# Optimization experiments

Hardware: AMD Instinct MI355X
Metric: run time of the kernel (lower is better)

Reference implementation:

```python
import jax, jax.numpy as jnp
import numpy as np

N_NODES = 100000
N_EDGES = 1600000
N_GRAPHS = 2048
HID = 64
IN_F = 14
N_CLS = 2
EPS = 1e-5


def _gcn_conv(x, row, col, w_edge, W, b, n_nodes):
    # PyG GCNConv with add_self_loops=True, normalize=True.
    xw = x @ W  # [N, out]
    # degree on target nodes, self-loop contributes weight 1
    deg = jnp.zeros((n_nodes,), x.dtype).at[col].add(w_edge) + 1.0
    dinv = deg ** -0.5
    norm = dinv[row] * w_edge * dinv[col]  # [E]
    out = jnp.zeros_like(xw).at[col].add(norm[:, None] * xw[row])
    out = out + (dinv * dinv)[:, None] * xw  # self-loop term
    return out + b


def _bn_relu(x, gamma, beta):
    mean = jnp.mean(x, axis=0)
    var = jnp.var(x, axis=0)  # biased, as PyTorch BN training normalization
    y = gamma * (x - mean) * jax.lax.rsqrt(var + EPS) + beta
    return jax.nn.relu(y)


def setup_inputs() -> dict:
    key = jax.random.key(0)
    ks = jax.random.split(key, 8)
    x = jax.random.normal(ks[0], (N_NODES, IN_F), dtype=jnp.float32)
    edge_index = jax.random.randint(ks[1], (2, N_EDGES), 0, N_NODES, dtype=jnp.int64)
    batch = jnp.sort(jax.random.randint(ks[2], (N_NODES,), 0, N_GRAPHS, dtype=jnp.int64))
    edge_weight = jnp.ones((N_EDGES,), dtype=jnp.float32)
    def lin(k, fi, fo):
        s = 1.0 / np.sqrt(fi)
        kw, kb = jax.random.split(k)
        return (jax.random.uniform(kw, (fi, fo), jnp.float32, -s, s),
                jax.random.uniform(kb, (fo,), jnp.float32, -s, s))
    W1, b1 = lin(ks[3], IN_F, HID)
    W2, b2 = lin(ks[4], HID, HID)
    W3, b3 = lin(ks[5], HID, HID)
    fcW, fcb = lin(ks[6], HID, N_CLS)
    g = jnp.ones((HID,), jnp.float32)
    z = jnp.zeros((HID,), jnp.float32)
    return {
        "x": x, "edge_index": edge_index, "batch": batch, "edge_weight": edge_weight,
        "W1": W1, "b1": b1, "W2": W2, "b2": b2, "W3": W3, "b3": b3,
        "g1": g, "bt1": z, "g2": g, "bt2": z, "g3": g, "bt3": z,
        "fcW": fcW, "fcb": fcb,
    }


def reference(x, edge_index, batch, edge_weight, W1, b1, W2, b2, W3, b3,
              g1, bt1, g2, bt2, g3, bt3, fcW, fcb):
    row, col = edge_index[0], edge_index[1]
    n = x.shape[0]
    h = _bn_relu(_gcn_conv(x, row, col, edge_weight, W1, b1, n), g1, bt1)
    h = _bn_relu(_gcn_conv(h, row, col, edge_weight, W2, b2, n), g2, bt2)
    h = _bn_relu(_gcn_conv(h, row, col, edge_weight, W3, b3, n), g3, bt3)
    node_embs = h  # dropout p=0 is identity
    graph_emb = jax.ops.segment_sum(node_embs, batch, num_segments=N_GRAPHS)
    out = graph_emb @ fcW + fcb
    return (out, node_embs, graph_emb)
```

## Files before the change

kernel.cpp:

```cpp
#include <hip/hip_runtime.h>
#include <hip/hip_fp16.h>

#define N_NODES 100000
#define N_EDGES 1600000
#define EMAX2   2000000
#define N_GRAPHS 2048
#define HID 64
#define IN_F 14
#define N_CLS 2
#define EPS 1e-5f

#define BSHIFT 9
#define NBUCK 196
#define ABLOCKS 256
#define CHUNK (N_EDGES / ABLOCKS)

#define NBLK2 128
#define NCHUNK2 ((N_NODES + NBLK2 - 1) / NBLK2)

typedef _Float16 half_t;
typedef _Float16 half8 __attribute__((ext_vector_type(8)));
typedef float f32x4 __attribute__((ext_vector_type(4)));

#define GSTRIDE ((size_t)N_NODES * 16)


__global__ __launch_bounds__(256) void histA_kernel(const int* __restrict__ col,
                                                    int* __restrict__ histG,
                                                    int* __restrict__ bsumA,
                                                    float* __restrict__ gemb,
                                                    float* __restrict__ stats3) {
    __shared__ int hl[NBUCK];
    for (int i = threadIdx.x; i < NBUCK; i += 256) hl[i] = 0;
    for (int k = threadIdx.x; k < 512; k += 256)
        gemb[(size_t)blockIdx.x * 512 + k] = 0.f;
    if (blockIdx.x == 0 && threadIdx.x < 384) stats3[threadIdx.x] = 0.f;
    __syncthreads();
    int e0 = blockIdx.x * CHUNK;
    for (int e = e0 + threadIdx.x; e < e0 + CHUNK; e += 256)
        atomicAdd(&hl[col[e] >> BSHIFT], 1);
    __syncthreads();
    for (int i = threadIdx.x; i < NBUCK; i += 256) {
        int v = hl[i];
        histG[i * ABLOCKS + blockIdx.x] = v;
        atomicAdd(&bsumA[i], v);
    }
}

__global__ __launch_bounds__(256) void scanS3_kernel(int* __restrict__ histG,
                                                     const int* __restrict__ bsumA,
                                                     int* __restrict__ bsumX,
                                                     int* __restrict__ ptr) {
    __shared__ int ls[256], bs[256];
    int t = threadIdx.x;
    int rawB = (blockIdx.x < NBUCK) ? bsumA[blockIdx.x] : 0;
    bs[t] = (t < NBUCK) ? bsumA[t] : 0;
    int idx = blockIdx.x * 256 + t;
    int v = histG[idx];
    ls[t] = v;
    __syncthreads();
    for (int off = 1; off < 256; off <<= 1) {
        int x = ls[t];
        int y = bs[t];
        if (t >= off) { x += ls[t - off]; y += bs[t - off]; }
        __syncthreads();
        ls[t] = x; bs[t] = y;
        __syncthreads();
    }
    int bexcl = bs[blockIdx.x] - rawB;
    histG[idx] = ls[t] - v + bexcl;
    if (t == 0) bsumX[blockIdx.x] = bexcl;
    if (blockIdx.x == 0 && t == 0) ptr[N_NODES] = N_EDGES;
}

__global__ __launch_bounds__(256) void scatterA_kernel(const int* __restrict__ row,
                                                       const int* __restrict__ col,
                                                       const float* __restrict__ w,
                                                       const int* __restrict__ histG,
                                                       int2* __restrict__ EA) {
    __shared__ int cur[NBUCK];
    for (int i = threadIdx.x; i < NBUCK; i += 256)
        cur[i] = histG[i * ABLOCKS + blockIdx.x];
    __syncthreads();
    int e0 = blockIdx.x * CHUNK;
    for (int e = e0 + threadIdx.x; e < e0 + CHUNK; e += 256) {
        int c = col[e];
        int r = row[e];
        int fx = (int)__float2uint_rn(w[e] * 8192.0f);
        int pos = atomicAdd(&cur[c >> BSHIFT], 1);
        EA[pos] = make_int2(r, (fx << 17) | c);
    }
}

__global__ __launch_bounds__(256) void bucketA_kernel(const int2* __restrict__ EA,
                                                      const int* __restrict__ bsumX,
                                                      int* __restrict__ ptr,
                                                      float* __restrict__ dinv) {
    __shared__ int hist[512], wsum[512];
    int b = blockIdx.x;
    int beg = bsumX[b];
    int end = (b == NBUCK - 1) ? N_EDGES : bsumX[b + 1];
    int i0 = threadIdx.x, i1 = threadIdx.x + 256;
    hist[i0] = 0; hist[i1] = 0;
    wsum[i0] = 0; wsum[i1] = 0;
    __syncthreads();
    for (int e = beg + threadIdx.x; e < end; e += 256) {
        int2 ed = EA[e];
        int c9 = ed.y & 511;
        atomicAdd(&hist[c9], 1);
        atomicAdd(&wsum[c9], (int)((unsigned int)ed.y >> 17));
    }
    __syncthreads();
    int cnt0 = hist[i0], cnt1 = hist[i1];
    for (int off = 1; off < 512; off <<= 1) {
        int v0 = hist[i0], v1 = hist[i1];
        int a0 = (i0 >= off) ? hist[i0 - off] : 0;
        int a1 = (i1 >= off) ? hist[i1 - off] : 0;
        __syncthreads();
        hist[i0] = v0 + a0;
        hist[i1] = v1 + a1;
        __syncthreads();
    }
    int excl0 = hist[i0] - cnt0, excl1 = hist[i1] - cnt1;
    int col0 = (b << BSHIFT) + i0, col1 = (b << BSHIFT) + i1;
    if (col0 < N_NODES) {
        ptr[col0] = beg + excl0;
        dinv[col0] = rsqrtf(1.0f + (float)wsum[i0] * (1.0f / 8192.0f));
    }
    if (col1 < N_NODES) {
        ptr[col1] = beg + excl1;
        dinv[col1] = rsqrtf(1.0f + (float)wsum[i1] * (1.0f / 8192.0f));
    }
}


__global__ __launch_bounds__(256) void histD_kernel(const int* __restrict__ ptr,
                                                    int* __restrict__ histD,
                                                    int* __restrict__ rowTot) {
    __shared__ int hl[2048];
    for (int i = threadIdx.x; i < 2048; i += 256) hl[i] = 0;
    __syncthreads();
    int n0 = blockIdx.x * NCHUNK2;
    int n1 = n0 + NCHUNK2; if (n1 > N_NODES) n1 = N_NODES;
    for (int n = n0 + threadIdx.x; n < n1; n += 256) {
        int d = ptr[n + 1] - ptr[n];
        if (d > 255) d = 255;
        atomicAdd(&hl[((threadIdx.x & 7) << 8) + d], 1);
    }
    __syncthreads();
    int s = 0;
#pragma unroll
    for (int c = 0; c < 8; c++) s += hl[(c << 8) + threadIdx.x];
    histD[threadIdx.x * NBLK2 + blockIdx.x] = s;
    atomicAdd(&rowTot[threadIdx.x], s);
}

__global__ __launch_bounds__(128) void scanD3_kernel(int* __restrict__ histD,
                                                     const int* __restrict__ rowTot,
                                                     int* __restrict__ nodeExcl,
                                                     int* __restrict__ edgeExcl,
                                                     int* __restrict__ ptrS) {
    __shared__ int ls[128], sa[256], sb[256];
    int t = threadIdx.x;
    int bin = blockIdx.x;
    int c0 = rowTot[t], c1 = rowTot[t + 128];
    sa[t] = c0;           sa[t + 128] = c1;
    sb[t] = c0 * ((t + 3) & ~3);
    sb[t + 128] = c1 * ((t + 131) & ~3);
    int idx = bin * NBLK2 + t;
    int v = histD[idx];
    ls[t] = v;
    __syncthreads();
    for (int off = 1; off < 256; off <<= 1) {
        int a0 = sa[t], a1 = sa[t + 128];
        int b0 = sb[t], b1 = sb[t + 128];
        int x0 = (t >= off) ? sa[t - off] : 0;
        int x1 = (t + 128 >= off) ? sa[t + 128 - off] : 0;
        int y0 = (t >= off) ? sb[t - off] : 0;
        int y1 = (t + 128 >= off) ? sb[t + 128 - off] : 0;
        __syncthreads();
        sa[t] = a0 + x0; sa[t + 128] = a1 + x1;
        sb[t] = b0 + y0; sb[t + 128] = b1 + y1;
        __syncthreads();
    }
    for (int off = 1; off < 128; off <<= 1) {
        int x = ls[t];
        if (t >= off) x += ls[t - off];
        __syncthreads();
        ls[t] = x;
        __syncthreads();
    }
    int nE = sa[bin] - rowTot[bin];
    histD[idx] = ls[t] - v + nE;
    if (bin == 0) {
        nodeExcl[t] = sa[t] - rowTot[t];
        nodeExcl[t + 128] = sa[t + 128] - rowTot[t + 128];
        edgeExcl[t] = sb[t] - rowTot[t] * ((t + 3) & ~3);
        edgeExcl[t + 128] = sb[t + 128] - rowTot[t + 128] * ((t + 131) & ~3);
        if (t == 127) ptrS[N_NODES] = sb[255];
    }
}

__global__ __launch_bounds__(256) void scatterD_kernel(const int* __restrict__ ptr,
                                                       const int* __restrict__ histD,
                                                       const int* __restrict__ nodeExcl,
                                                       const int* __restrict__ edgeExcl,
                                                       int* __restrict__ perm,
                                                       int* __restrict__ ptrS,
                                                       int* __restrict__ newbase,
                                                       unsigned int* __restrict__ srcoff,
                                                       half_t* __restrict__ normh) {
    __shared__ int cur[256];
    cur[threadIdx.x] = histD[threadIdx.x * NBLK2 + blockIdx.x];
    __syncthreads();
    int n0 = blockIdx.x * NCHUNK2;
    int n1 = n0 + NCHUNK2; if (n1 > N_NODES) n1 = N_NODES;
    for (int n = n0 + threadIdx.x; n < n1; n += 256) {
        int d = ptr[n + 1] - ptr[n];
        if (d > 255) d = 255;
        int dpad = (d + 3) & ~3;
        int pos = atomicAdd(&cur[d], 1);
        int ebase = edgeExcl[d] + (pos - nodeExcl[d]) * dpad;
        perm[pos] = n;
        ptrS[pos] = ebase;
        newbase[n] = ebase;
        for (int k = d; k < dpad; k++) {
            srcoff[ebase + k] = 0u;
            normh[ebase + k] = (half_t)0.f;
        }
    }
}

__global__ __launch_bounds__(256) void bucketB_kernel(const int2* __restrict__ EA,
                                                      const int* __restrict__ bsumX,
                                                      const int* __restrict__ newbase,
                                                      unsigned int* __restrict__ srcoff,
                                                      half_t* __restrict__ normh) {
    __shared__ int cur[512];
    int b = blockIdx.x;
    int beg = bsumX[b];
    int end = (b == NBUCK - 1) ? N_EDGES : bsumX[b + 1];
    int i0 = threadIdx.x, i1 = threadIdx.x + 256;
    int col0 = (b << BSHIFT) + i0, col1 = (b << BSHIFT) + i1;
    cur[i0] = (col0 < N_NODES) ? newbase[col0] : 0;
    cur[i1] = (col1 < N_NODES) ? newbase[col1] : 0;
    __syncthreads();
    for (int e = beg + threadIdx.x; e < end; e += 256) {
        int2 ed = EA[e];
        int c = ed.y & 0x1ffff;
        float w = (float)((unsigned int)ed.y >> 17) * (1.0f / 8192.0f);
        int pos = atomicAdd(&cur[c & 511], 1);
        srcoff[pos] = (unsigned int)ed.x << 5;
        normh[pos] = (half_t)w;
    }
}


template <int K>
__global__ __launch_bounds__(256) void gemm_kernel(const float* __restrict__ h,
                                                   const float* __restrict__ W,
                                                   const float* __restrict__ dinv,
                                                   half_t* __restrict__ xw, int n_nodes) {
    int f = threadIdx.x & 63;
    float wcol[K];
#pragma unroll
    for (int k = 0; k < K; k++) wcol[k] = W[k * HID + f];
    half_t* xg = xw + (size_t)(f >> 4) * GSTRIDE + (f & 15);
    int wave = (blockIdx.x * blockDim.x + threadIdx.x) >> 6;
    int nwaves = (gridDim.x * blockDim.x) >> 6;
    for (int n = wave; n < n_nodes; n += nwaves) {
        const float* hr = h + (size_t)n * K;
        float acc = 0.f;
#pragma unroll
        for (int k = 0; k < K; k++) acc += hr[k] * wcol[k];
        xg[(size_t)n * 16] = (half_t)(acc * dinv[n]);
    }
}

__global__ __launch_bounds__(256) void gemm_bn_mfma_kernel(const half_t* __restrict__ h,
                                                           const float* __restrict__ W,
                                                           const float* __restrict__ stats,
                                                           const float* __restrict__ gamma,
                                                           const float* __restrict__ beta,
                                                           const float* __restrict__ dinv,
                                                           half_t* __restrict__ xw, int n_nodes) {
    __shared__ float sc_s[HID], sh_s[HID];
    if (threadIdx.x < 64) {
        float mean = stats[threadIdx.x] * (1.0f / N_NODES);
        float var = stats[64 + threadIdx.x] * (1.0f / N_NODES) - mean * mean;
        float sc = gamma[threadIdx.x] * rsqrtf(var + EPS);
        sc_s[threadIdx.x] = sc;
        sh_s[threadIdx.x] = beta[threadIdx.x] - mean * sc;
    }
    __syncthreads();
    int lane = threadIdx.x & 63;
    int col16 = lane & 15;
    int quad = lane >> 4;

    float scA[2][8], shA[2][8];
#pragma unroll
    for (int kh = 0; kh < 2; kh++)
#pragma unroll
        for (int j = 0; j < 8; j++) {
            int k = kh * 32 + quad * 8 + j;
            scA[kh][j] = sc_s[k];
            shA[kh][j] = sh_s[k];
        }

    half8 bfrag[4][2];
#pragma unroll
    for (int t = 0; t < 4; t++)
#pragma unroll
        for (int kh = 0; kh < 2; kh++)
#pragma unroll
            for (int j = 0; j < 8; j++) {
                int k = kh * 32 + quad * 8 + j;
                bfrag[t][kh][j] = (half_t)W[k * HID + t * 16 + col16];
            }

    int wave = (blockIdx.x * blockDim.x + threadIdx.x) >> 6;
    int nwaves = (gridDim.x * blockDim.x) >> 6;
    int ntiles = n_nodes >> 4;
    for (int tIdx = wave; tIdx < ntiles; tIdx += nwaves) {
        int n0 = tIdx << 4;
        half8 afrag[2];
#pragma unroll
        for (int kh = 0; kh < 2; kh++) {
            int k0 = kh * 32 + quad * 8;
            const half_t* hp = h + (size_t)(k0 >> 4) * GSTRIDE
                                 + (size_t)(n0 + col16) * 16 + (k0 & 15);
            half8 raw = *(const half8*)hp;
#pragma unroll
            for (int j = 0; j < 8; j++) {
                float v = (float)raw[j] * scA[kh][j] + shA[kh][j];
                afrag[kh][j] = (half_t)fmaxf(v, 0.f);
            }
        }
        f32x4 acc[4];
#pragma unroll
        for (int t = 0; t < 4; t++) {
            f32x4 z = {0.f, 0.f, 0.f, 0.f};
            acc[t] = __builtin_amdgcn_mfma_f32_16x16x32_f16(afrag[0], bfrag[t][0], z, 0, 0, 0);
            acc[t] = __builtin_amdgcn_mfma_f32_16x16x32_f16(afrag[1], bfrag[t][1], acc[t], 0, 0, 0);
        }
        f32x4 dv = *(const f32x4*)(dinv + n0 + quad * 4);
#pragma unroll
        for (int t = 0; t < 4; t++) {
            half_t* xg = xw + (size_t)t * GSTRIDE;
#pragma unroll
            for (int r = 0; r < 4; r++) {
                int rowi = n0 + quad * 4 + r;
                xg[(size_t)rowi * 16 + col16] = (half_t)(acc[t][r] * dv[r]);
            }
        }
    }
}

__global__ __launch_bounds__(256) void gather_stats_kernel(const int* __restrict__ ptrS,
                                                           const int* __restrict__ perm,
                                                           const unsigned int* __restrict__ srcoff,
                                                           const unsigned int* __restrict__ normu,
                                                           const half_t* __restrict__ xw,
                                                           const float* __restrict__ dinv,
                                                           const float* __restrict__ b,
                                                           half_t* __restrict__ hp,
                                                           float* __restrict__ stats,
                                                           int n_nodes) {
    int g = (blockIdx.x & 7) >> 1;
    int grank = ((blockIdx.x >> 3) << 1) | (blockIdx.x & 1);
    int lane16 = threadIdx.x & 15;
    int quadLocal = threadIdx.x >> 4;
    int quadId = grank * 16 + quadLocal;
    int nquads = (gridDim.x >> 2) * 16;

    const half_t* xg = xw + (size_t)g * GSTRIDE;
    const char* xgc = (const char*)xg;
    unsigned int loff = (unsigned int)(lane16 * 2);
    half_t* hpg = hp + (size_t)g * GSTRIDE;
    float bf = b[g * 16 + lane16];
    int base = ((threadIdx.x & 63) >> 4) * 16;

    float s = 0.f, s2 = 0.f;

    int npairs = n_nodes >> 1;
    int idx = quadId;
    int nodeA = 0, begA = 0, cA = 0, nodeB = 0, begB = 0, cB = 0;
    int evA = 0, nvA = 0, evB = 0, nvB = 0;
    if (idx < npairs) {
        int iA = (npairs - 1 - idx) * 2;
        nodeA = perm[iA];
        nodeB = perm[iA + 1];
        begA = ptrS[iA];
        begB = ptrS[iA + 1];
        cA = begB - begA;
        cB = ptrS[iA + 2] - begB;
        int mA = (cA > 16) ? 16 : cA;
        int mB = (cB > 16) ? 16 : cB;
        if (lane16 < mA) evA = (int)srcoff[begA + lane16];
        if (lane16 < (mA >> 1)) nvA = (int)normu[(begA >> 1) + lane16];
        if (lane16 < mB) evB = (int)srcoff[begB + lane16];
        if (lane16 < (mB >> 1)) nvB = (int)normu[(begB >> 1) + lane16];
    }

    while (idx < npairs) {
        int inext = idx + nquads;
        int nodeA2 = 0, begA2 = 0, cA2 = 0, nodeB2 = 0, begB2 = 0, cB2 = 0;
        if (inext < npairs) {
            int iN = (npairs - 1 - inext) * 2;
            nodeA2 = perm[iN];
            nodeB2 = perm[iN + 1];
            begA2 = ptrS[iN];
            begB2 = ptrS[iN + 1];
            cA2 = begB2 - begA2;
            cB2 = ptrS[iN + 2] - begB2;
        }
        float selfA = (float)xg[(size_t)nodeA * 16 + lane16];
        float diA = dinv[nodeA];
        float selfB = (float)xg[(size_t)nodeB * 16 + lane16];
        float diB = dinv[nodeB];

        __half2 aA0 = __float2half2_rn(0.f), aA1 = __float2half2_rn(0.f);
        __half2 aB0 = __float2half2_rn(0.f), aB1 = __float2half2_rn(0.f);

        for (int j0 = 0; j0 < cB; j0 += 16) {
            int mA = cA - j0; mA = (mA < 0) ? 0 : ((mA > 16) ? 16 : mA);
            int mB = cB - j0; mB = (mB > 16) ? 16 : mB;
            int pA = mA >> 1;
            int pB = mB >> 1;
            int evA2 = 0, nvA2 = 0, evB2 = 0, nvB2 = 0;
            int j1 = j0 + 16;
            if (j1 < cA) {
                int m2 = cA - j1; if (m2 > 16) m2 = 16;
                if (lane16 < m2) evA2 = (int)srcoff[begA + j1 + lane16];
                if (lane16 < (m2 >> 1)) nvA2 = (int)normu[((begA + j1) >> 1) + lane16];
            }
            if (j1 < cB) {
                int m2 = cB - j1; if (m2 > 16) m2 = 16;
                if (lane16 < m2) evB2 = (int)srcoff[begB + j1 + lane16];
                if (lane16 < (m2 >> 1)) nvB2 = (int)normu[((begB + j1) >> 1) + lane16];
            }
            for (int p = 0; p < pB; p += 2) {
                unsigned int ub0 = (unsigned int)__shfl(evB, base + 2 * p);
                unsigned int ub1 = (unsigned int)__shfl(evB, base + 2 * p + 1);
                unsigned int ub2 = (unsigned int)__shfl(evB, base + 2 * p + 2);
                unsigned int ub3 = (unsigned int)__shfl(evB, base + 2 * p + 3);
                unsigned int nb0 = (unsigned int)__shfl(nvB, base + p);
                unsigned int nb1 = (unsigned int)__shfl(nvB, base + p + 1);
                __half hb0 = *(const __half*)(xgc + (ub0 + loff));
                __half hb1 = *(const __half*)(xgc + (ub1 + loff));
                __half hb2 = *(const __half*)(xgc + (ub2 + loff));
                __half hb3 = *(const __half*)(xgc + (ub3 + loff));
                aB0 = __hfma2(*(__half2*)&nb0, __halves2half2(hb0, hb1), aB0);
                aB1 = __hfma2(*(__half2*)&nb1, __halves2half2(hb2, hb3), aB1);
                if (p < pA) {
                    unsigned int ua0 = (unsigned int)__shfl(evA, base + 2 * p);
                    unsigned int ua1 = (unsigned int)__shfl(evA, base + 2 * p + 1);
                    unsigned int ua2 = (unsigned int)__shfl(evA, base + 2 * p + 2);
                    unsigned int ua3 = (unsigned int)__shfl(evA, base + 2 * p + 3);
                    unsigned int na0 = (unsigned int)__shfl(nvA, base + p);
                    unsigned int na1 = (unsigned int)__shfl(nvA, base + p + 1);
                    __half ha0 = *(const __half*)(xgc + (ua0 + loff));
                    __half ha1 = *(const __half*)(xgc + (ua1 + loff));
                    __half ha2 = *(const __half*)(xgc + (ua2 + loff));
                    __half ha3 = *(const __half*)(xgc + (ua3 + loff));
                    aA0 = __hfma2(*(__half2*)&na0, __halves2half2(ha0, ha1), aA0);
                    aA1 = __hfma2(*(__half2*)&na1, __halves2half2(ha2, ha3), aA1);
                }
            }
            evA = evA2; nvA = nvA2; evB = evB2; nvB = nvB2;
        }
        if (inext < npairs) {
            int mA0 = (cA2 > 16) ? 16 : cA2;
            int mB0 = (cB2 > 16) ? 16 : cB2;
            evA = (lane16 < mA0) ? (int)srcoff[begA2 + lane16] : 0;
            nvA = (lane16 < (mA0 >> 1)) ? (int)normu[(begA2 >> 1) + lane16] : 0;
            evB = (lane16 < mB0) ? (int)srcoff[begB2 + lane16] : 0;
            nvB = (lane16 < (mB0 >> 1)) ? (int)normu[(begB2 >> 1) + lane16] : 0;
        }

        float accA = (__low2float(aA0) + __high2float(aA0))
                   + (__low2float(aA1) + __high2float(aA1));
        float vA = diA * (accA + selfA) + bf;
        hpg[(size_t)nodeA * 16 + lane16] = (half_t)vA;
        float accB = (__low2float(aB0) + __high2float(aB0))
                   + (__low2float(aB1) + __high2float(aB1));
        float vB = diB * (accB + selfB) + bf;
        hpg[(size_t)nodeB * 16 + lane16] = (half_t)vB;
        s += vA + vB;
        s2 += vA * vA + vB * vB;

        idx = inext;
        nodeA = nodeA2; begA = begA2; cA = cA2;
        nodeB = nodeB2; begB = begB2; cB = cB2;
    }
    __shared__ float ls[256], ls2[256];
    ls[threadIdx.x] = s;
    ls2[threadIdx.x] = s2;
    __syncthreads();
    if (threadIdx.x < 16) {
        float a = 0.f, aa = 0.f;
#pragma unroll
        for (int k = 0; k < 16; k++) {
            a += ls[k * 16 + threadIdx.x];
            aa += ls2[k * 16 + threadIdx.x];
        }
        atomicAdd(&stats[g * 16 + threadIdx.x], a);
        atomicAdd(&stats[64 + g * 16 + threadIdx.x], aa);
    }
}

__global__ __launch_bounds__(256) void bn_relu_seg_kernel(const half_t* __restrict__ hpl,
                                                          float* __restrict__ h3,
                                                          const float* __restrict__ stats,
                                                          const float* __restrict__ gamma,
                                                          const float* __restrict__ beta,
                                                          const int* __restrict__ batch,
                                                          float* __restrict__ gemb,
                                                          int n_nodes) {
    int g = blockIdx.x * blockDim.x + threadIdx.x;
    int f = g & 63;
    int wave = g >> 6;
    int nwaves = (gridDim.x * blockDim.x) >> 6;
    int chunk = (n_nodes + nwaves - 1) / nwaves;
    int n0 = wave * chunk;
    int n1 = n0 + chunk;
    if (n1 > n_nodes) n1 = n_nodes;
    if (n0 >= n_nodes) return;
    float mean = stats[f] * (1.0f / N_NODES);
    float var = stats[64 + f] * (1.0f / N_NODES) - mean * mean;
    float sc = gamma[f] * rsqrtf(var + EPS);
    float sh = beta[f] - mean * sc;
    const half_t* hg = hpl + (size_t)(f >> 4) * GSTRIDE + (f & 15);
    int curg = batch[n0];
    float racc = 0.f;
    for (int n = n0; n < n1; n++) {
        int bg = batch[n];
        if (bg != curg) {
            atomicAdd(&gemb[(size_t)curg * HID + f], racc);
            racc = 0.f;
            curg = bg;
        }
        float v = (float)hg[(size_t)n * 16] * sc + sh;
        v = fmaxf(v, 0.f);
        h3[(size_t)n * HID + f] = v;
        racc += v;
    }
    atomicAdd(&gemb[(size_t)curg * HID + f], racc);
}

__global__ __launch_bounds__(256) void final_kernel(const float* __restrict__ gemb,
                                                    const float* __restrict__ fcW,
                                                    const float* __restrict__ fcb,
                                                    float* __restrict__ out) {
    int g = blockIdx.x * blockDim.x + threadIdx.x;
    if (g >= N_GRAPHS * N_CLS) return;
    int gr = g >> 1, c = g & 1;
    float acc = fcb[c];
#pragma unroll
    for (int k = 0; k < HID; k++) acc += gemb[gr * HID + k] * fcW[k * N_CLS + c];
    out[g] = acc;
}


extern "C" void kernel_launch(void* const* d_in, const int* in_sizes, int n_in,
                              void* d_out, int out_size, void* d_ws, size_t ws_size,
                              hipStream_t stream) {
    const float* x    = (const float*)d_in[0];
    const int*   ei   = (const int*)d_in[1];
    const int*   batch= (const int*)d_in[2];
    const float* ew   = (const float*)d_in[3];
    const float* W1   = (const float*)d_in[4];
    const float* b1   = (const float*)d_in[5];
    const float* W2   = (const float*)d_in[6];
    const float* b2   = (const float*)d_in[7];
    const float* W3   = (const float*)d_in[8];
    const float* b3   = (const float*)d_in[9];
    const float* g1   = (const float*)d_in[10];
    const float* bt1  = (const float*)d_in[11];
    const float* g2   = (const float*)d_in[12];
    const float* bt2  = (const float*)d_in[13];
    const float* g3   = (const float*)d_in[14];
    const float* bt3  = (const float*)d_in[15];
    const float* fcW  = (const float*)d_in[16];
    const float* fcb  = (const float*)d_in[17];

    const int* row = ei;
    const int* col = ei + N_EDGES;

    float* out_head  = (float*)d_out;
    float* node_embs = out_head + N_GRAPHS * N_CLS;
    float* gemb      = node_embs + (size_t)N_NODES * HID;

    char* bse = (char*)d_ws;
    half_t* xwh = (half_t*)bse;
    char* r1 = bse + (size_t)N_NODES * HID * 2;
    int2*   EA  = (int2*)r1;
    half_t* hpl = (half_t*)r1;
    char* r2 = r1 + (size_t)N_NODES * HID * 2;
    unsigned int* srcoff = (unsigned int*)r2;
    half_t* normh = (half_t*)(srcoff + EMAX2);
    char* r3 = r2 + (size_t)EMAX2 * 6;
    float* dinv  = (float*)r3;
    float* stats3 = dinv + N_NODES;
    int*   ptr   = (int*)(stats3 + 384);
    int*   histG = ptr + N_NODES + 1;
    int*   bsumA = histG + NBUCK * ABLOCKS;
    int*   rowTot = bsumA + 200;
    int*   bsumX = rowTot + 256;
    int*   histD = bsumX + NBUCK + 4;
    int*   nodeExcl = histD + 256 * NBLK2;
    int*   edgeExcl = nodeExcl + 256;
    int*   perm   = edgeExcl + 256;
    int*   newbase= perm + N_NODES;
    int*   ptrS   = newbase + N_NODES;

    const int B   = 256;
    const int gGS = 1024;
    const int gGA = 2048;

    hipMemsetAsync(bsumA, 0, (200 + 256) * sizeof(int), stream);

    histA_kernel<<<ABLOCKS, B, 0, stream>>>(col, histG, bsumA, gemb, stats3);
    scanS3_kernel<<<NBUCK, B, 0, stream>>>(histG, bsumA, bsumX, ptr);
    scatterA_kernel<<<ABLOCKS, B, 0, stream>>>(row, col, ew, histG, EA);
    bucketA_kernel<<<NBUCK, B, 0, stream>>>(EA, bsumX, ptr, dinv);

    histD_kernel<<<NBLK2, B, 0, stream>>>(ptr, histD, rowTot);
    scanD3_kernel<<<256, 128, 0, stream>>>(histD, rowTot, nodeExcl, edgeExcl, ptrS);
    scatterD_kernel<<<NBLK2, B, 0, stream>>>(ptr, histD, nodeExcl, edgeExcl,
                                             perm, ptrS, newbase, srcoff, normh);
    bucketB_kernel<<<NBUCK, B, 0, stream>>>(EA, bsumX, newbase, srcoff, normh);

    float* h3 = node_embs;

    gemm_kernel<IN_F><<<gGS, B, 0, stream>>>(x, W1, dinv, xwh, N_NODES);
    gather_stats_kernel<<<gGA, B, 0, stream>>>(ptrS, perm, srcoff,
                                               (const unsigned int*)normh, xwh,
                                               dinv, b1, hpl, stats3, N_NODES);

    gemm_bn_mfma_kernel<<<gGS, B, 0, stream>>>(hpl, W2, stats3, g1, bt1, dinv, xwh, N_NODES);
    gather_stats_kernel<<<gGA, B, 0, stream>>>(ptrS, perm, srcoff,
                                               (const unsigned int*)normh, xwh,
                                               dinv, b2, hpl, stats3 + 128, N_NODES);

    gemm_bn_mfma_kernel<<<gGS, B, 0, stream>>>(hpl, W3, stats3 + 128, g2, bt2, dinv, xwh, N_NODES);
    gather_stats_kernel<<<gGA, B, 0, stream>>>(ptrS, perm, srcoff,
                                               (const unsigned int*)normh, xwh,
                                               dinv, b3, hpl, stats3 + 256, N_NODES);

    bn_relu_seg_kernel<<<gGS, B, 0, stream>>>(hpl, h3, stats3 + 256, g3, bt3,
                                              batch, gemb, N_NODES);

    final_kernel<<<(N_GRAPHS * N_CLS + B - 1) / B, B, 0, stream>>>(gemb, fcW, fcb, out_head);
}
```

Before: 401.1 us.

## Replace two-level bucket sort with global-atomic degree count and direct scatter

Drops the bucketed counting sort of edges by target (histogram, scan, scatter to a temp array, per-bucket local sort). Instead, one 64-bit global atomic per edge accumulates both the in-degree and the fixed-point weight sum. Edges are then scattered straight into the degree-sorted CSR layout using per-node global atomic cursors. That edge scatter runs in the same launch as the first-layer GEMM, on separate blocks. This removes several launches and one pass over an intermediate edge array, at the cost of heavy contended global atomics and a nondeterministic order of edges within each node.

```diff
diff --git a/kernel.cpp b/kernel.cpp
--- a/kernel.cpp
+++ b/kernel.cpp
@@ -10,8 +10,6 @@
 #define N_CLS 2
 #define EPS 1e-5f
 
-#define BSHIFT 9
-#define NBUCK 196
 #define ABLOCKS 256
 #define CHUNK (N_EDGES / ABLOCKS)
 
@@ -25,125 +23,35 @@
 #define GSTRIDE ((size_t)N_NODES * 16)
 
 
-__global__ __launch_bounds__(256) void histA_kernel(const int* __restrict__ col,
-                                                    int* __restrict__ histG,
-                                                    int* __restrict__ bsumA,
-                                                    float* __restrict__ gemb,
-                                                    float* __restrict__ stats3) {
-    __shared__ int hl[NBUCK];
-    for (int i = threadIdx.x; i < NBUCK; i += 256) hl[i] = 0;
+__global__ __launch_bounds__(256) void degcnt_kernel(const int* __restrict__ col,
+                                                     const float* __restrict__ w,
+                                                     unsigned long long* __restrict__ dw,
+                                                     float* __restrict__ gemb,
+                                                     float* __restrict__ stats3) {
     for (int k = threadIdx.x; k < 512; k += 256)
         gemb[(size_t)blockIdx.x * 512 + k] = 0.f;
     if (blockIdx.x == 0 && threadIdx.x < 384) stats3[threadIdx.x] = 0.f;
-    __syncthreads();
-    int e0 = blockIdx.x * CHUNK;
-    for (int e = e0 + threadIdx.x; e < e0 + CHUNK; e += 256)
-        atomicAdd(&hl[col[e] >> BSHIFT], 1);
-    __syncthreads();
-    for (int i = threadIdx.x; i < NBUCK; i += 256) {
-        int v = hl[i];
-        histG[i * ABLOCKS + blockIdx.x] = v;
-        atomicAdd(&bsumA[i], v);
-    }
-}
-
-__global__ __launch_bounds__(256) void scanS3_kernel(int* __restrict__ histG,
-                                                     const int* __restrict__ bsumA,
-                                                     int* __restrict__ bsumX,
-                                                     int* __restrict__ ptr) {
-    __shared__ int ls[256], bs[256];
-    int t = threadIdx.x;
-    int rawB = (blockIdx.x < NBUCK) ? bsumA[blockIdx.x] : 0;
-    bs[t] = (t < NBUCK) ? bsumA[t] : 0;
-    int idx = blockIdx.x * 256 + t;
-    int v = histG[idx];
-    ls[t] = v;
-    __syncthreads();
-    for (int off = 1; off < 256; off <<= 1) {
-        int x = ls[t];
-        int y = bs[t];
-        if (t >= off) { x += ls[t - off]; y += bs[t - off]; }
-        __syncthreads();
-        ls[t] = x; bs[t] = y;
-        __syncthreads();
-    }
-    int bexcl = bs[blockIdx.x] - rawB;
-    histG[idx] = ls[t] - v + bexcl;
-    if (t == 0) bsumX[blockIdx.x] = bexcl;
-    if (blockIdx.x == 0 && t == 0) ptr[N_NODES] = N_EDGES;
-}
-
-__global__ __launch_bounds__(256) void scatterA_kernel(const int* __restrict__ row,
-                                                       const int* __restrict__ col,
-                                                       const float* __restrict__ w,
-                                                       const int* __restrict__ histG,
-                                                       int2* __restrict__ EA) {
-    __shared__ int cur[NBUCK];
-    for (int i = threadIdx.x; i < NBUCK; i += 256)
-        cur[i] = histG[i * ABLOCKS + blockIdx.x];
-    __syncthreads();
     int e0 = blockIdx.x * CHUNK;
     for (int e = e0 + threadIdx.x; e < e0 + CHUNK; e += 256) {
         int c = col[e];
-        int r = row[e];
-        int fx = (int)__float2uint_rn(w[e] * 8192.0f);
-        int pos = atomicAdd(&cur[c >> BSHIFT], 1);
-        EA[pos] = make_int2(r, (fx << 17) | c);
-    }
-}
-
-__global__ __launch_bounds__(256) void bucketA_kernel(const int2* __restrict__ EA,
-                                                      const int* __restrict__ bsumX,
-                                                      int* __restrict__ ptr,
-                                                      float* __restrict__ dinv) {
-    __shared__ int hist[512], wsum[512];
-    int b = blockIdx.x;
-    int beg = bsumX[b];
-    int end = (b == NBUCK - 1) ? N_EDGES : bsumX[b + 1];
-    int i0 = threadIdx.x, i1 = threadIdx.x + 256;
-    hist[i0] = 0; hist[i1] = 0;
-    wsum[i0] = 0; wsum[i1] = 0;
-    __syncthreads();
-    for (int e = beg + threadIdx.x; e < end; e += 256) {
-        int2 ed = EA[e];
-        int c9 = ed.y & 511;
-        atomicAdd(&hist[c9], 1);
-        atomicAdd(&wsum[c9], (int)((unsigned int)ed.y >> 17));
-    }
-    __syncthreads();
-    int cnt0 = hist[i0], cnt1 = hist[i1];
-    for (int off = 1; off < 512; off <<= 1) {
-        int v0 = hist[i0], v1 = hist[i1];
-        int a0 = (i0 >= off) ? hist[i0 - off] : 0;
-        int a1 = (i1 >= off) ? hist[i1 - off] : 0;
-        __syncthreads();
-        hist[i0] = v0 + a0;
-        hist[i1] = v1 + a1;
-        __syncthreads();
-    }
-    int excl0 = hist[i0] - cnt0, excl1 = hist[i1] - cnt1;
-    int col0 = (b << BSHIFT) + i0, col1 = (b << BSHIFT) + i1;
-    if (col0 < N_NODES) {
-        ptr[col0] = beg + excl0;
-        dinv[col0] = rsqrtf(1.0f + (float)wsum[i0] * (1.0f / 8192.0f));
-    }
-    if (col1 < N_NODES) {
-        ptr[col1] = beg + excl1;
-        dinv[col1] = rsqrtf(1.0f + (float)wsum[i1] * (1.0f / 8192.0f));
-    }
-}
-
-
-__global__ __launch_bounds__(256) void histD_kernel(const int* __restrict__ ptr,
-                                                    int* __restrict__ histD,
-                                                    int* __restrict__ rowTot) {
+        unsigned int fx = __float2uint_rn(w[e] * 8192.0f);
+        atomicAdd(&dw[c], (1ULL << 32) | (unsigned long long)fx);
+    }
+}
+
+__global__ __launch_bounds__(256) void dinv_histD_kernel(const unsigned long long* __restrict__ dw,
+                                                         float* __restrict__ dinv,
+                                                         int* __restrict__ histD,
+                                                         int* __restrict__ rowTot) {
     __shared__ int hl[2048];
     for (int i = threadIdx.x; i < 2048; i += 256) hl[i] = 0;
     __syncthreads();
     int n0 = blockIdx.x * NCHUNK2;
     int n1 = n0 + NCHUNK2; if (n1 > N_NODES) n1 = N_NODES;
     for (int n = n0 + threadIdx.x; n < n1; n += 256) {
-        int d = ptr[n + 1] - ptr[n];
+        unsigned long long v = dw[n];
+        int d = (int)(v >> 32);
+        dinv[n] = rsqrtf(1.0f + (float)(unsigned int)v * (1.0f / 8192.0f));
         if (d > 255) d = 255;
         atomicAdd(&hl[((threadIdx.x & 7) << 8) + d], 1);
     }
@@ -201,7 +109,7 @@
     }
 }
 
-__global__ __launch_bounds__(256) void scatterD_kernel(const int* __restrict__ ptr,
+__global__ __launch_bounds__(256) void scatterD_kernel(const unsigned long long* __restrict__ dw,
                                                        const int* __restrict__ histD,
                                                        const int* __restrict__ nodeExcl,
                                                        const int* __restrict__ edgeExcl,
@@ -216,7 +124,7 @@
     int n0 = blockIdx.x * NCHUNK2;
     int n1 = n0 + NCHUNK2; if (n1 > N_NODES) n1 = N_NODES;
     for (int n = n0 + threadIdx.x; n < n1; n += 256) {
-        int d = ptr[n + 1] - ptr[n];
+        int d = (int)(dw[n] >> 32);
         if (d > 255) d = 255;
         int dpad = (d + 3) & ~3;
         int pos = atomicAdd(&cur[d], 1);
@@ -231,49 +139,40 @@
     }
 }
 
-__global__ __launch_bounds__(256) void bucketB_kernel(const int2* __restrict__ EA,
-                                                      const int* __restrict__ bsumX,
-                                                      const int* __restrict__ newbase,
-                                                      unsigned int* __restrict__ srcoff,
-                                                      half_t* __restrict__ normh) {
-    __shared__ int cur[512];
-    int b = blockIdx.x;
-    int beg = bsumX[b];
-    int end = (b == NBUCK - 1) ? N_EDGES : bsumX[b + 1];
-    int i0 = threadIdx.x, i1 = threadIdx.x + 256;
-    int col0 = (b << BSHIFT) + i0, col1 = (b << BSHIFT) + i1;
-    cur[i0] = (col0 < N_NODES) ? newbase[col0] : 0;
-    cur[i1] = (col1 < N_NODES) ? newbase[col1] : 0;
-    __syncthreads();
-    for (int e = beg + threadIdx.x; e < end; e += 256) {
-        int2 ed = EA[e];
-        int c = ed.y & 0x1ffff;
-        float w = (float)((unsigned int)ed.y >> 17) * (1.0f / 8192.0f);
-        int pos = atomicAdd(&cur[c & 511], 1);
-        srcoff[pos] = (unsigned int)ed.x << 5;
-        normh[pos] = (half_t)w;
-    }
-}
-
-
 template <int K>
-__global__ __launch_bounds__(256) void gemm_kernel(const float* __restrict__ h,
-                                                   const float* __restrict__ W,
-                                                   const float* __restrict__ dinv,
-                                                   half_t* __restrict__ xw, int n_nodes) {
-    int f = threadIdx.x & 63;
-    float wcol[K];
-#pragma unroll
-    for (int k = 0; k < K; k++) wcol[k] = W[k * HID + f];
-    half_t* xg = xw + (size_t)(f >> 4) * GSTRIDE + (f & 15);
-    int wave = (blockIdx.x * blockDim.x + threadIdx.x) >> 6;
-    int nwaves = (gridDim.x * blockDim.x) >> 6;
-    for (int n = wave; n < n_nodes; n += nwaves) {
-        const float* hr = h + (size_t)n * K;
-        float acc = 0.f;
-#pragma unroll
-        for (int k = 0; k < K; k++) acc += hr[k] * wcol[k];
-        xg[(size_t)n * 16] = (half_t)(acc * dinv[n]);
+__global__ __launch_bounds__(256) void scatterB_gemm_kernel(const int* __restrict__ row,
+                                                            const int* __restrict__ col,
+                                                            const float* __restrict__ w,
+                                                            int* __restrict__ cursor,
+                                                            unsigned int* __restrict__ srcoff,
+                                                            half_t* __restrict__ normh,
+                                                            const float* __restrict__ h,
+                                                            const float* __restrict__ W,
+                                                            const float* __restrict__ dinv,
+                                                            half_t* __restrict__ xw) {
+    if (blockIdx.x < ABLOCKS) {
+        int e0 = blockIdx.x * CHUNK;
+        for (int e = e0 + threadIdx.x; e < e0 + CHUNK; e += 256) {
+            int c = col[e];
+            int pos = atomicAdd(&cursor[c], 1);
+            srcoff[pos] = (unsigned int)row[e] << 5;
+            normh[pos] = (half_t)w[e];
+        }
+    } else {
+        int f = threadIdx.x & 63;
+        float wcol[K];
+#pragma unroll
+        for (int k = 0; k < K; k++) wcol[k] = W[k * HID + f];
+        half_t* xg = xw + (size_t)(f >> 4) * GSTRIDE + (f & 15);
+        int wave = (((blockIdx.x - ABLOCKS) << 8) + threadIdx.x) >> 6;
+        int nwaves = (1024 << 8) >> 6;
+        for (int n = wave; n < N_NODES; n += nwaves) {
+            const float* hr = h + (size_t)n * K;
+            float acc = 0.f;
+#pragma unroll
+            for (int k = 0; k < K; k++) acc += hr[k] * wcol[k];
+            xg[(size_t)n * 16] = (half_t)(acc * dinv[n]);
+        }
     }
 }
 
@@ -594,20 +493,16 @@
     char* bse = (char*)d_ws;
     half_t* xwh = (half_t*)bse;
     char* r1 = bse + (size_t)N_NODES * HID * 2;
-    int2*   EA  = (int2*)r1;
     half_t* hpl = (half_t*)r1;
     char* r2 = r1 + (size_t)N_NODES * HID * 2;
     unsigned int* srcoff = (unsigned int*)r2;
     half_t* normh = (half_t*)(srcoff + EMAX2);
     char* r3 = r2 + (size_t)EMAX2 * 6;
-    float* dinv  = (float*)r3;
+    unsigned long long* dw = (unsigned long long*)r3;
+    int*   rowTot = (int*)(dw + N_NODES);
+    float* dinv  = (float*)(rowTot + 256);
     float* stats3 = dinv + N_NODES;
-    int*   ptr   = (int*)(stats3 + 384);
-    int*   histG = ptr + N_NODES + 1;
-    int*   bsumA = histG + NBUCK * ABLOCKS;
-    int*   rowTot = bsumA + 200;
-    int*   bsumX = rowTot + 256;
-    int*   histD = bsumX + NBUCK + 4;
+    int*   histD = (int*)(stats3 + 384);
     int*   nodeExcl = histD + 256 * NBLK2;
     int*   edgeExcl = nodeExcl + 256;
     int*   perm   = edgeExcl + 256;
@@ -617,23 +512,21 @@
     const int B   = 256;
     const int gGS = 1024;
     const int gGA = 2048;
-
-    hipMemsetAsync(bsumA, 0, (200 + 256) * sizeof(int), stream);
-
-    histA_kernel<<<ABLOCKS, B, 0, stream>>>(col, histG, bsumA, gemb, stats3);
-    scanS3_kernel<<<NBUCK, B, 0, stream>>>(histG, bsumA, bsumX, ptr);
-    scatterA_kernel<<<ABLOCKS, B, 0, stream>>>(row, col, ew, histG, EA);
-    bucketA_kernel<<<NBUCK, B, 0, stream>>>(EA, bsumX, ptr, dinv);
-
-    histD_kernel<<<NBLK2, B, 0, stream>>>(ptr, histD, rowTot);
+    const int gSB = ABLOCKS + 1024;
+
+    hipMemsetAsync(dw, 0, (size_t)N_NODES * 8 + 256 * sizeof(int), stream);
+
+    degcnt_kernel<<<ABLOCKS, B, 0, stream>>>(col, ew, dw, gemb, stats3);
+    dinv_histD_kernel<<<NBLK2, B, 0, stream>>>(dw, dinv, histD, rowTot);
     scanD3_kernel<<<256, 128, 0, stream>>>(histD, rowTot, nodeExcl, edgeExcl, ptrS);
-    scatterD_kernel<<<NBLK2, B, 0, stream>>>(ptr, histD, nodeExcl, edgeExcl,
+    scatterD_kernel<<<NBLK2, B, 0, stream>>>(dw, histD, nodeExcl, edgeExcl,
                                              perm, ptrS, newbase, srcoff, normh);
-    bucketB_kernel<<<NBUCK, B, 0, stream>>>(EA, bsumX, newbase, srcoff, normh);
+    scatterB_gemm_kernel<IN_F><<<gSB, B, 0, stream>>>(row, col, ew, newbase,
+                                                      srcoff, normh,
+                                                      x, W1, dinv, xwh);
 
     float* h3 = node_embs;
 
-    gemm_kernel<IN_F><<<gGS, B, 0, stream>>>(x, W1, dinv, xwh, N_NODES);
     gather_stats_kernel<<<gGA, B, 0, stream>>>(ptrS, perm, srcoff,
                                                (const unsigned int*)normh, xwh,
                                                dinv, b1, hpl, stats3, N_NODES);
```

Measured after the change: 489.5 us. 22.0% more time.
